# Performance work log

Measured on AMD Instinct MI355X. Metric: run time of the kernel, lower is better.

Reference implementation:

```python
import jax, jax.numpy as jnp
import numpy as np

B, N, D, H = 2, 2048, 1024, 16
HD = D // H
SCALE = 1.0 / float(np.sqrt(HD))


def _cx(r, i):
    return (r + 1j * i).astype(jnp.complex64)


def setup_inputs() -> dict:
    key = jax.random.key(0)
    ks = jax.random.split(key, 20)
    inp = {
        "Z_r": jax.random.normal(ks[0], (B, N, D), jnp.float32),
        "Z_i": jax.random.normal(ks[1], (B, N, D), jnp.float32),
    }
    i = 2
    w_scale = 0.02
    for nm in ("q", "k", "v", "o"):
        inp[f"w{nm}_r"] = jax.random.normal(ks[i], (D, D), jnp.float32) * w_scale
        inp[f"w{nm}_i"] = jax.random.normal(ks[i + 1], (D, D), jnp.float32) * w_scale
        inp[f"b{nm}_r"] = jax.random.normal(ks[i + 2], (D,), jnp.float32) * w_scale
        inp[f"b{nm}_i"] = jax.random.normal(ks[i + 3], (D,), jnp.float32) * w_scale
        i += 4
    inp["mask"] = jax.random.randint(ks[18], (B, N), 0, 2, jnp.int32)
    return inp


def reference(Z_r, Z_i, wq_r, wq_i, bq_r, bq_i, wk_r, wk_i, bk_r, bk_i,
              wv_r, wv_i, bv_r, bv_i, wo_r, wo_i, bo_r, bo_i, mask):
    Z = _cx(Z_r, Z_i)  # (B,N,D) complex64

    def lin(x, wr, wi, br, bi):  # complex nn.Linear: x @ W^T + b
        return x @ _cx(wr, wi).T + _cx(br, bi)

    def heads(x):  # (B,N,D) -> (B,H,N,HD)
        return x.reshape(B, N, H, HD).transpose(0, 2, 1, 3)

    q = heads(lin(Z, wq_r, wq_i, bq_r, bq_i))
    k = heads(lin(Z, wk_r, wk_i, bk_r, bk_i))
    v = heads(lin(Z, wv_r, wv_i, bv_r, bv_i))

    # Re(q @ k^T) with plain transpose (no conjugate), as in the torch code:
    # Re = qr.kr^T - qi.ki^T  (computed directly on real parts, no wasted imag GEMM)
    scores = (jnp.einsum('bhnd,bhmd->bhnm', q.real, k.real)
              - jnp.einsum('bhnd,bhmd->bhnm', q.imag, k.imag)) * SCALE
    scores = jnp.where(mask[:, None, None, :] == 0, jnp.float32(-1e9), scores)
    w = jax.nn.softmax(scores, axis=-1)  # (B,H,N,N) real

    # complex output: real weights times complex V -> apply to real/imag separately
    out_r = jnp.einsum('bhnm,bhmd->bhnd', w, v.real)
    out_i = jnp.einsum('bhnm,bhmd->bhnd', w, v.imag)
    out = _cx(out_r, out_i).transpose(0, 2, 1, 3).reshape(B, N, D)

    y = Z + lin(out, wo_r, wo_i, bo_r, bo_i)
    # return real/imag stacked as float32: (2,B,N,D)
    return jnp.stack([y.real, y.imag])
```

## Files before the change

kernel.cpp:

```cpp
#include <hip/hip_runtime.h>
#include <math.h>

#define BB 2
#define NN 2048
#define DD 1024
#define KA 2048
#define HH 16
#define HD 64
#define MM (BB*NN)
#define SCALE 0.125f

typedef __attribute__((ext_vector_type(8))) short bf16x8;
typedef __attribute__((ext_vector_type(4))) short bf16x4;
typedef __attribute__((ext_vector_type(4))) float f32x4;

#define MFMA(a,b,c) __builtin_amdgcn_mfma_f32_16x16x32_bf16(a,b,c,0,0,0)

__device__ __forceinline__ unsigned short f2bf(float x) {
    union { float f; unsigned u; } v; v.f = x;
    unsigned r = v.u + 0x7FFFu + ((v.u >> 16) & 1u);
    return (unsigned short)(r >> 16);
}

__device__ __forceinline__ void async16(void* l, const void* g) {
    __builtin_amdgcn_global_load_lds(
        (const __attribute__((address_space(1))) unsigned int*)g,
        (__attribute__((address_space(3))) unsigned int*)l, 16, 0, 0);
}

__device__ __forceinline__ bf16x8 ld8s(const short* p) {
    bf16x4 lo = *(const bf16x4*)p;
    bf16x4 hi = *(const bf16x4*)(p + 4);
    bf16x8 r;
    r[0]=lo[0]; r[1]=lo[1]; r[2]=lo[2]; r[3]=lo[3];
    r[4]=hi[0]; r[5]=hi[1]; r[6]=hi[2]; r[7]=hi[3];
    return r;
}
__device__ __forceinline__ void st8s(short* p, bf16x8 v) {
    bf16x4 lo, hi;
    lo[0]=v[0]; lo[1]=v[1]; lo[2]=v[2]; lo[3]=v[3];
    hi[0]=v[4]; hi[1]=v[5]; hi[2]=v[6]; hi[3]=v[7];
    *(bf16x4*)p = lo;
    *(bf16x4*)(p + 4) = hi;
}

__global__ __launch_bounds__(256) void mask_scan(const int* __restrict__ mask,
                                                 int* __restrict__ idxArr,
                                                 int* __restrict__ cntArr)
{
    const int b = blockIdx.x, t = threadIdx.x;
    __shared__ int part[256];
    int m[8]; int c = 0;
#pragma unroll
    for (int j = 0; j < 8; j++) { m[j] = mask[b*NN + t*8 + j]; c += (m[j] != 0); }
    part[t] = c; __syncthreads();
    for (int off = 1; off < 256; off <<= 1) {
        int v = (t >= off) ? part[t - off] : 0;
        __syncthreads();
        part[t] += v;
        __syncthreads();
    }
    int base = part[t] - c;
    int total = part[255];
#pragma unroll
    for (int j = 0; j < 8; j++) if (m[j]) idxArr[b*NN + base++] = t*8 + j;
    for (int p = total + t; p < NN; p += 256) idxArr[b*NN + p] = 0;
    if (t == 0) cntArr[b] = total;
}

__global__ __launch_bounds__(256) void cvt_aug(
    const float* __restrict__ Zr, const float* __restrict__ Zi,
    const float* __restrict__ wqr, const float* __restrict__ wqi,
    const float* __restrict__ wkr, const float* __restrict__ wki,
    const float* __restrict__ wvr, const float* __restrict__ wvi,
    const float* __restrict__ wor, const float* __restrict__ woi,
    unsigned short* __restrict__ Zaug,
    unsigned short* __restrict__ Wqa, unsigned short* __restrict__ Wka,
    unsigned short* __restrict__ Wva, unsigned short* __restrict__ Woa)
{
    const int bid = blockIdx.x, t = threadIdx.x;
    const int col = t * 8;
    const float* src;
    float sgn = 1.0f;
    unsigned short* dst;

    if (bid < 4096) {
        const int m = bid;
        src = (col < 1024) ? (Zr + (size_t)m*1024 + col) : (Zi + (size_t)m*1024 + col - 1024);
        dst = Zaug + (size_t)m * KA + col;
    } else {
        const int w = (bid - 4096) >> 11;
        const int r = (bid - 4096) & 2047;
        const int o = r & 1023;
        const float *wr_, *wi_;
        unsigned short* wa;
        switch (w) {
            case 0: wr_ = wqr; wi_ = wqi; wa = Wqa; break;
            case 1: wr_ = wkr; wi_ = wki; wa = Wka; break;
            case 2: wr_ = wvr; wi_ = wvi; wa = Wva; break;
            default: wr_ = wor; wi_ = woi; wa = Woa; break;
        }
        const bool imagrow = (r >= 1024);
        if (!imagrow) {
            if (col < 1024) { src = wr_ + (size_t)o*1024 + col; sgn = 1.0f; }
            else            { src = wi_ + (size_t)o*1024 + col - 1024; sgn = -1.0f; }
        } else {
            const float s = (w == 1) ? -1.0f : 1.0f;
            if (col < 1024) { src = wi_ + (size_t)o*1024 + col; sgn = s; }
            else            { src = wr_ + (size_t)o*1024 + col - 1024; sgn = s; }
        }
        dst = wa + (size_t)r * KA + col;
    }

    float4 a = *(const float4*)src;
    float4 b4 = *(const float4*)(src + 4);
    bf16x8 o8;
    o8[0]=(short)f2bf(sgn*a.x); o8[1]=(short)f2bf(sgn*a.y);
    o8[2]=(short)f2bf(sgn*a.z); o8[3]=(short)f2bf(sgn*a.w);
    o8[4]=(short)f2bf(sgn*b4.x); o8[5]=(short)f2bf(sgn*b4.y);
    o8[6]=(short)f2bf(sgn*b4.z); o8[7]=(short)f2bf(sgn*b4.w);
    *(bf16x8*)dst = o8;
}

__global__ __launch_bounds__(256) void proj_all(
    const unsigned short* __restrict__ Zaug,
    const unsigned short* __restrict__ Wqa, const unsigned short* __restrict__ Wka,
    const unsigned short* __restrict__ Wva,
    const float* __restrict__ bqr, const float* __restrict__ bqi,
    const float* __restrict__ bkr, const float* __restrict__ bki,
    const float* __restrict__ bvr, const float* __restrict__ bvi,
    const int* __restrict__ idxArr, const int* __restrict__ cntArr,
    unsigned short* __restrict__ Qr, unsigned short* __restrict__ Qi,
    unsigned short* __restrict__ Krc, unsigned short* __restrict__ nKic,
    unsigned short* __restrict__ Vtr, unsigned short* __restrict__ Vti)
{
    const int gx = blockIdx.x;
    int slice, b = 0, m0c;
    const unsigned short* wsel;
    const float *br, *bi;
    if (gx < 32) {
        slice = 0; m0c = gx * 128;
        wsel = Wqa; br = bqr; bi = bqi;
    } else if (gx < 64) {
        slice = 1; int t = gx - 32; b = t >> 4; m0c = (t & 15) * 128;
        wsel = Wka; br = bkr; bi = bki;
    } else {
        slice = 2; int t = gx - 64; b = t >> 4; m0c = (t & 15) * 128;
        wsel = Wva; br = bvr; bi = bvi;
    }
    if (slice != 0) {
        const int cnt = cntArr[b];
        if (m0c >= ((cnt + 63) & ~63)) return;
    }

    __shared__ __align__(16) short S[2][2][128][32];
    __shared__ int idx_s[128];

    const int tid = threadIdx.x;
    const int lane = tid & 63, wave = tid >> 6;
    const int lr = lane & 15, lg = lane >> 4;
    const int wrow = (wave >> 1) * 64, wcol = (wave & 1) * 64;
    const int o0 = blockIdx.y * 128;

    if (tid < 128)
        idx_s[tid] = (slice == 0) ? (m0c + tid) : (b*NN + idxArr[b*NN + m0c + tid]);
    __syncthreads();

    const int rsub = lane >> 2;
    const int colo = (lane & 3) * 8;

    const unsigned short* gp[4];
    gp[0] = Zaug + (size_t)idx_s[wave*16 + rsub] * KA + colo;
    gp[1] = Zaug + (size_t)idx_s[(wave + 4)*16 + rsub] * KA + colo;
    gp[2] = wsel + (size_t)(o0 + wave*16 + rsub) * KA + colo;
    gp[3] = wsel + (size_t)(o0 + 64 + wave*16 + rsub) * KA + colo;

    int lpo[4];
    lpo[0] = wave * 1024 + lane * 16;
    lpo[1] = (wave + 4) * 1024 + lane * 16;
    lpo[2] = 8192 + wave * 1024 + lane * 16;
    lpo[3] = 8192 + (wave + 4) * 1024 + lane * 16;

    f32x4 acc[4][4];
#pragma unroll
    for (int m = 0; m < 4; m++)
#pragma unroll
        for (int n = 0; n < 4; n++) acc[m][n] = (f32x4){0.f,0.f,0.f,0.f};

#pragma unroll
    for (int i = 0; i < 4; i++) { async16((char*)S + lpo[i], gp[i]); gp[i] += 32; }
    asm volatile("s_waitcnt vmcnt(0)" ::: "memory");
    __builtin_amdgcn_s_barrier();
    __builtin_amdgcn_sched_barrier(0);

    for (int t = 0; t < KA/32; t++) {
        const int cur = t & 1;
        char* nb = (char*)S + (cur ^ 1) * 16384;
#pragma unroll
        for (int i = 0; i < 4; i++) { async16(nb + lpo[i], gp[i]); gp[i] += 32; }

        const short (*Sa)[32] = (const short (*)[32])((const char*)S + cur * 16384);
        const short (*Sb)[32] = Sa + 128;
        bf16x8 af[4], bw[4];
#pragma unroll
        for (int m = 0; m < 4; m++) af[m] = *(const bf16x8*)&Sa[wrow + m*16 + lr][lg*8];
#pragma unroll
        for (int n = 0; n < 4; n++) bw[n] = *(const bf16x8*)&Sb[wcol + n*16 + lr][lg*8];
#pragma unroll
        for (int m = 0; m < 4; m++)
#pragma unroll
            for (int n = 0; n < 4; n++) acc[m][n] = MFMA(af[m], bw[n], acc[m][n]);

        asm volatile("s_waitcnt vmcnt(0)" ::: "memory");
        __builtin_amdgcn_s_barrier();
        __builtin_amdgcn_sched_barrier(0);
    }

#pragma unroll
    for (int mi = 0; mi < 4; mi++)
#pragma unroll
        for (int nj = 0; nj < 4; nj++) {
            const int o = o0 + wcol + nj*16 + lr;
            const int half = o >> 10;
            const int oc = o & 1023;
            const int h = oc >> 6, hd = oc & 63;
            const float bias = half ? ((slice == 1) ? -bi[oc] : bi[oc]) : br[oc];
            if (slice == 2) {
                bf16x4 p4;
#pragma unroll
                for (int reg = 0; reg < 4; reg++)
                    p4[reg] = (short)f2bf(acc[mi][nj][reg] + bias);
                const int jc = m0c + wrow + mi*16 + lg*4;
                size_t base = ((size_t)((b*HH + h)*HD + hd)) * NN + jc;
                if (half) *(bf16x4*)&Vti[base] = p4;
                else      *(bf16x4*)&Vtr[base] = p4;
            } else if (slice == 1) {
                unsigned short* dst = half ? nKic : Krc;
#pragma unroll
                for (int reg = 0; reg < 4; reg++) {
                    const int jc = m0c + wrow + mi*16 + lg*4 + reg;
                    dst[((size_t)((b*HH + h)*NN + jc)) * HD + hd] =
                        f2bf(acc[mi][nj][reg] + bias);
                }
            } else {
                unsigned short* dst = half ? Qi : Qr;
#pragma unroll
                for (int reg = 0; reg < 4; reg++) {
                    const int m = m0c + wrow + mi*16 + lg*4 + reg;
                    const int b2 = m >> 11, n = m & (NN - 1);
                    dst[((size_t)((b2*HH + h)*NN + n)) * HD + hd] =
                        f2bf((acc[mi][nj][reg] + bias) * SCALE);
                }
            }
        }
}

#define LDP 72
__global__ __launch_bounds__(256) void attn_mfma(
    const unsigned short* __restrict__ Qr, const unsigned short* __restrict__ Qi,
    const unsigned short* __restrict__ Krc, const unsigned short* __restrict__ nKic,
    const unsigned short* __restrict__ Vtc, const unsigned short* __restrict__ Vtic,
    const int* __restrict__ cntArr,
    unsigned short* __restrict__ Aaug)
{
    __shared__ short Kr_s[64][LDP], Ki_s[64][LDP], Vr_s[64][LDP], Vi_s[64][LDP];
    __shared__ short P_s[4][32][LDP];

    const int tid = threadIdx.x;
    const int lane = tid & 63, wave = tid >> 6;
    const int lr = lane & 15, lg = lane >> 4;
    const int h = blockIdx.y, b = blockIdx.z;
    const int n0 = blockIdx.x * 128 + wave * 32;
    const size_t qb = ((size_t)(b*HH + h)) * NN * HD;
    const int cnt = cntArr[b];
    const int ct = (cnt + 63) & ~63;

    bf16x8 qr[2][2], qi[2][2];
#pragma unroll
    for (int mf = 0; mf < 2; mf++)
#pragma unroll
        for (int kf = 0; kf < 2; kf++) {
            qr[mf][kf] = *(const bf16x8*)&Qr[qb + (size_t)(n0 + mf*16 + lr) * HD + kf*32 + lg*8];
            qi[mf][kf] = *(const bf16x8*)&Qi[qb + (size_t)(n0 + mf*16 + lr) * HD + kf*32 + lg*8];
        }

    f32x4 o_r[2][4], o_i[2][4];
#pragma unroll
    for (int mf = 0; mf < 2; mf++)
#pragma unroll
        for (int nf = 0; nf < 4; nf++) {
            o_r[mf][nf] = (f32x4){0.f,0.f,0.f,0.f};
            o_i[mf][nf] = (f32x4){0.f,0.f,0.f,0.f};
        }
    float m_run[2][4], l_run[2][4];
#pragma unroll
    for (int mf = 0; mf < 2; mf++)
#pragma unroll
        for (int r = 0; r < 4; r++) { m_run[mf][r] = -3.0e38f; l_run[mf][r] = 0.0f; }

    for (int t0 = 0; t0 < ct; t0 += 64) {
        __syncthreads();
        for (int c = tid; c < 512; c += 256) {
            int row = c >> 3, ch = (c & 7) * 8;
            st8s(&Kr_s[row][ch], *(const bf16x8*)&Krc [qb + (size_t)(t0 + row) * HD + ch]);
            st8s(&Ki_s[row][ch], *(const bf16x8*)&nKic[qb + (size_t)(t0 + row) * HD + ch]);
            st8s(&Vr_s[row][ch], *(const bf16x8*)&Vtc [qb + (size_t)row * NN + t0 + ch]);
            st8s(&Vi_s[row][ch], *(const bf16x8*)&Vtic[qb + (size_t)row * NN + t0 + ch]);
        }
        __syncthreads();

        f32x4 sacc[2][4];
#pragma unroll
        for (int nf = 0; nf < 4; nf++) {
            bf16x8 k0f = ld8s(&Kr_s[nf*16 + lr][lg*8]);
            bf16x8 k1f = ld8s(&Kr_s[nf*16 + lr][32 + lg*8]);
            bf16x8 i0f = ld8s(&Ki_s[nf*16 + lr][lg*8]);
            bf16x8 i1f = ld8s(&Ki_s[nf*16 + lr][32 + lg*8]);
#pragma unroll
            for (int mf = 0; mf < 2; mf++) {
                f32x4 a = (f32x4){0.f,0.f,0.f,0.f};
                a = MFMA(qr[mf][0], k0f, a);
                a = MFMA(qr[mf][1], k1f, a);
                a = MFMA(qi[mf][0], i0f, a);
                a = MFMA(qi[mf][1], i1f, a);
                sacc[mf][nf] = a;
            }
        }

        if (t0 + 64 > cnt) {
#pragma unroll
            for (int nf = 0; nf < 4; nf++) {
                if (t0 + nf*16 + lr >= cnt) {
#pragma unroll
                    for (int mf = 0; mf < 2; mf++)
#pragma unroll
                        for (int r = 0; r < 4; r++) sacc[mf][nf][r] = -1e9f;
                }
            }
        }

#pragma unroll
        for (int mf = 0; mf < 2; mf++) {
            float fac[4];
#pragma unroll
            for (int r = 0; r < 4; r++) {
                float v = fmaxf(fmaxf(sacc[mf][0][r], sacc[mf][1][r]),
                                fmaxf(sacc[mf][2][r], sacc[mf][3][r]));
                v = fmaxf(v, __shfl_xor(v, 1, 64));
                v = fmaxf(v, __shfl_xor(v, 2, 64));
                v = fmaxf(v, __shfl_xor(v, 4, 64));
                v = fmaxf(v, __shfl_xor(v, 8, 64));
                float mn = fmaxf(m_run[mf][r], v);
                fac[r] = __expf(m_run[mf][r] - mn);
                m_run[mf][r] = mn;
            }
            float psum[4] = {0.f, 0.f, 0.f, 0.f};
#pragma unroll
            for (int nf = 0; nf < 4; nf++)
#pragma unroll
                for (int r = 0; r < 4; r++) {
                    float p = __expf(sacc[mf][nf][r] - m_run[mf][r]);
                    psum[r] += p;
                    P_s[wave][mf*16 + lg*4 + r][nf*16 + lr] = (short)f2bf(p);
                }
#pragma unroll
            for (int r = 0; r < 4; r++) {
                float ps = psum[r];
                ps += __shfl_xor(ps, 1, 64);
                ps += __shfl_xor(ps, 2, 64);
                ps += __shfl_xor(ps, 4, 64);
                ps += __shfl_xor(ps, 8, 64);
                l_run[mf][r] = l_run[mf][r] * fac[r] + ps;
            }
#pragma unroll
            for (int nf = 0; nf < 4; nf++)
#pragma unroll
                for (int r = 0; r < 4; r++) {
                    o_r[mf][nf][r] *= fac[r];
                    o_i[mf][nf][r] *= fac[r];
                }
        }
        __syncthreads();

        bf16x8 pa[2][2];
#pragma unroll
        for (int mf = 0; mf < 2; mf++) {
            pa[mf][0] = ld8s(&P_s[wave][mf*16 + lr][lg*8]);
            pa[mf][1] = ld8s(&P_s[wave][mf*16 + lr][32 + lg*8]);
        }
#pragma unroll
        for (int nf = 0; nf < 4; nf++) {
            bf16x8 v0 = ld8s(&Vr_s[nf*16 + lr][lg*8]);
            bf16x8 v1 = ld8s(&Vr_s[nf*16 + lr][32 + lg*8]);
            bf16x8 w0 = ld8s(&Vi_s[nf*16 + lr][lg*8]);
            bf16x8 w1 = ld8s(&Vi_s[nf*16 + lr][32 + lg*8]);
#pragma unroll
            for (int mf = 0; mf < 2; mf++) {
                o_r[mf][nf] = MFMA(pa[mf][0], v0, o_r[mf][nf]);
                o_r[mf][nf] = MFMA(pa[mf][1], v1, o_r[mf][nf]);
                o_i[mf][nf] = MFMA(pa[mf][0], w0, o_i[mf][nf]);
                o_i[mf][nf] = MFMA(pa[mf][1], w1, o_i[mf][nf]);
            }
        }
    }

#pragma unroll
    for (int mf = 0; mf < 2; mf++) {
        float invl[4];
#pragma unroll
        for (int r = 0; r < 4; r++) invl[r] = 1.0f / l_run[mf][r];
#pragma unroll
        for (int nf = 0; nf < 4; nf++)
#pragma unroll
            for (int r = 0; r < 4; r++) {
                int row = n0 + mf*16 + lg*4 + r;
                int col = h*HD + nf*16 + lr;
                size_t o = ((size_t)(b*NN + row)) * KA + col;
                Aaug[o]        = f2bf(o_r[mf][nf][r] * invl[r]);
                Aaug[o + 1024] = f2bf(o_i[mf][nf][r] * invl[r]);
            }
    }
}

__global__ __launch_bounds__(256) void final_mfma(
    const unsigned short* __restrict__ Aaug, const unsigned short* __restrict__ Woa,
    const float* __restrict__ bor, const float* __restrict__ boi,
    const float* __restrict__ Zr, const float* __restrict__ Zi,
    float* __restrict__ out)
{
    __shared__ __align__(16) short S[2][2][128][32];

    const int tid = threadIdx.x;
    const int lane = tid & 63, wave = tid >> 6;
    const int lr = lane & 15, lg = lane >> 4;
    const int wrow = (wave >> 1) * 64, wcol = (wave & 1) * 64;
    const int m0 = blockIdx.x * 128, o0 = blockIdx.y * 128;

    const int rsub = lane >> 2;
    const int colo = (lane & 3) * 8;

    const unsigned short* gp[4];
    gp[0] = Aaug + (size_t)(m0 + wave*16 + rsub) * KA + colo;
    gp[1] = Aaug + (size_t)(m0 + 64 + wave*16 + rsub) * KA + colo;
    gp[2] = Woa + (size_t)(o0 + wave*16 + rsub) * KA + colo;
    gp[3] = Woa + (size_t)(o0 + 64 + wave*16 + rsub) * KA + colo;

    int lpo[4];
    lpo[0] = wave * 1024 + lane * 16;
    lpo[1] = (wave + 4) * 1024 + lane * 16;
    lpo[2] = 8192 + wave * 1024 + lane * 16;
    lpo[3] = 8192 + (wave + 4) * 1024 + lane * 16;

    f32x4 acc[4][4];
#pragma unroll
    for (int m = 0; m < 4; m++)
#pragma unroll
        for (int n = 0; n < 4; n++) acc[m][n] = (f32x4){0.f,0.f,0.f,0.f};

#pragma unroll
    for (int i = 0; i < 4; i++) { async16((char*)S + lpo[i], gp[i]); gp[i] += 32; }
    asm volatile("s_waitcnt vmcnt(0)" ::: "memory");
    __builtin_amdgcn_s_barrier();
    __builtin_amdgcn_sched_barrier(0);

    for (int t = 0; t < KA/32; t++) {
        const int cur = t & 1;
        char* nb = (char*)S + (cur ^ 1) * 16384;
#pragma unroll
        for (int i = 0; i < 4; i++) { async16(nb + lpo[i], gp[i]); gp[i] += 32; }

        const short (*Sa)[32] = (const short (*)[32])((const char*)S + cur * 16384);
        const short (*Sb)[32] = Sa + 128;
        bf16x8 af[4], bw[4];
#pragma unroll
        for (int m = 0; m < 4; m++) af[m] = *(const bf16x8*)&Sa[wrow + m*16 + lr][lg*8];
#pragma unroll
        for (int n = 0; n < 4; n++) bw[n] = *(const bf16x8*)&Sb[wcol + n*16 + lr][lg*8];
#pragma unroll
        for (int m = 0; m < 4; m++)
#pragma unroll
            for (int n = 0; n < 4; n++) acc[m][n] = MFMA(af[m], bw[n], acc[m][n]);

        asm volatile("s_waitcnt vmcnt(0)" ::: "memory");
        __builtin_amdgcn_s_barrier();
        __builtin_amdgcn_sched_barrier(0);
    }

#pragma unroll
    for (int mi = 0; mi < 4; mi++)
#pragma unroll
        for (int nj = 0; nj < 4; nj++) {
            const int o = o0 + wcol + nj*16 + lr;
            const int half = o >> 10;
            const int oc = o & 1023;
            const float bias = half ? boi[oc] : bor[oc];
            const float* resid = half ? Zi : Zr;
            float* dst = out + (half ? (size_t)MM * DD : 0);
#pragma unroll
            for (int reg = 0; reg < 4; reg++) {
                const int m = m0 + wrow + mi*16 + lg*4 + reg;
                size_t zi = (size_t)m * DD + oc;
                dst[zi] = acc[mi][nj][reg] + bias + resid[zi];
            }
        }
}

extern "C" void kernel_launch(void* const* d_in, const int* in_sizes, int n_in,
                              void* d_out, int out_size, void* d_ws, size_t ws_size,
                              hipStream_t stream)
{
    const float* Zr  = (const float*)d_in[0];
    const float* Zi  = (const float*)d_in[1];
    const float* wqr = (const float*)d_in[2];
    const float* wqi = (const float*)d_in[3];
    const float* bqr = (const float*)d_in[4];
    const float* bqi = (const float*)d_in[5];
    const float* wkr = (const float*)d_in[6];
    const float* wki = (const float*)d_in[7];
    const float* bkr = (const float*)d_in[8];
    const float* bki = (const float*)d_in[9];
    const float* wvr = (const float*)d_in[10];
    const float* wvi = (const float*)d_in[11];
    const float* bvr = (const float*)d_in[12];
    const float* bvi = (const float*)d_in[13];
    const float* wor = (const float*)d_in[14];
    const float* woi = (const float*)d_in[15];
    const float* bor = (const float*)d_in[16];
    const float* boi = (const float*)d_in[17];
    const int*  mask = (const int*)d_in[18];

    unsigned short* w16 = (unsigned short*)d_ws;
    const size_t ZA = (size_t)MM * KA;
    const size_t WA = (size_t)KA * KA;
    const size_t HN = (size_t)MM * DD;
    unsigned short* Zaug = w16;
    unsigned short* Wqa  = Zaug + ZA;
    unsigned short* Wka  = Wqa + WA;
    unsigned short* Wva  = Wka + WA;
    unsigned short* Woa  = Wva + WA;
    unsigned short* Qr16 = Woa + WA;
    unsigned short* Qi16 = Qr16 + HN;
    unsigned short* Krc16 = Qi16 + HN;
    unsigned short* nKic16 = Krc16 + HN;
    unsigned short* Vtr16 = nKic16 + HN;
    unsigned short* Vti16 = Vtr16 + HN;
    unsigned short* Aaug = Vti16 + HN;
    int* idxArr = (int*)(Aaug + ZA);
    int* cntArr = idxArr + BB * NN;

    mask_scan<<<BB, 256, 0, stream>>>(mask, idxArr, cntArr);

    cvt_aug<<<12288, 256, 0, stream>>>(
        Zr, Zi, wqr, wqi, wkr, wki, wvr, wvi, wor, woi,
        Zaug, Wqa, Wka, Wva, Woa);

    proj_all<<<dim3(96, 16), 256, 0, stream>>>(
        Zaug, Wqa, Wka, Wva,
        bqr, bqi, bkr, bki, bvr, bvi, idxArr, cntArr,
        Qr16, Qi16, Krc16, nKic16, Vtr16, Vti16);

    attn_mfma<<<dim3(NN/128, HH, BB), 256, 0, stream>>>(
        Qr16, Qi16, Krc16, nKic16, Vtr16, Vti16, cntArr, Aaug);

    final_mfma<<<dim3(32, 16), 256, 0, stream>>>(
        Aaug, Woa, bor, boi, Zr, Zi, (float*)d_out);
}
```

Measured before the change: 309.5 us.

## Triple-buffer LDS in projection GEMMs with XOR-swizzled tiles to avoid bank conflicts

After: 266.3 us. -14.0%, faster.

```diff
diff --git a/kernel.cpp b/kernel.cpp
--- a/kernel.cpp
+++ b/kernel.cpp
@@ -9,6 +9,7 @@
 #define HD 64
 #define MM (BB*NN)
 #define SCALE 0.125f
+#define NT (KA/32)
 
 typedef __attribute__((ext_vector_type(8))) short bf16x8;
 typedef __attribute__((ext_vector_type(4))) short bf16x4;
@@ -153,7 +154,7 @@
         if (m0c >= ((cnt + 63) & ~63)) return;
     }
 
-    __shared__ __align__(16) short S[2][2][128][32];
+    __shared__ __align__(16) short S[3][2][128][32];
     __shared__ int idx_s[128];
 
     const int tid = threadIdx.x;
@@ -167,19 +168,23 @@
     __syncthreads();
 
     const int rsub = lane >> 2;
-    const int colo = (lane & 3) * 8;
+    const int csrc = (((lane & 3) ^ ((lane >> 3) & 3)) * 8);
 
     const unsigned short* gp[4];
-    gp[0] = Zaug + (size_t)idx_s[wave*16 + rsub] * KA + colo;
-    gp[1] = Zaug + (size_t)idx_s[(wave + 4)*16 + rsub] * KA + colo;
-    gp[2] = wsel + (size_t)(o0 + wave*16 + rsub) * KA + colo;
-    gp[3] = wsel + (size_t)(o0 + 64 + wave*16 + rsub) * KA + colo;
-
     int lpo[4];
-    lpo[0] = wave * 1024 + lane * 16;
-    lpo[1] = (wave + 4) * 1024 + lane * 16;
-    lpo[2] = 8192 + wave * 1024 + lane * 16;
-    lpo[3] = 8192 + (wave + 4) * 1024 + lane * 16;
+#pragma unroll
+    for (int i = 0; i < 4; i++) {
+        const int s = i * 4 + wave;
+        if (s < 8) {
+            const int row = s * 16 + rsub;
+            gp[i] = Zaug + (size_t)idx_s[row] * KA + csrc;
+            lpo[i] = s * 1024 + lane * 16;
+        } else {
+            const int row = (s - 8) * 16 + rsub;
+            gp[i] = wsel + (size_t)(o0 + row) * KA + csrc;
+            lpo[i] = 8192 + (s - 8) * 1024 + lane * 16;
+        }
+    }
 
     f32x4 acc[4][4];
 #pragma unroll
@@ -189,31 +194,53 @@
 
 #pragma unroll
     for (int i = 0; i < 4; i++) { async16((char*)S + lpo[i], gp[i]); gp[i] += 32; }
+#pragma unroll
+    for (int i = 0; i < 4; i++) { async16((char*)S + 16384 + lpo[i], gp[i]); gp[i] += 32; }
+
+    const int kb = ((lg ^ ((lr >> 1) & 3)) * 8);
+
+    int cur = 0, stg = 2;
+    for (int t = 0; t < NT - 1; t++) {
+        asm volatile("s_waitcnt vmcnt(4)" ::: "memory");
+        __builtin_amdgcn_s_barrier();
+        __builtin_amdgcn_sched_barrier(0);
+
+        if (t + 2 < NT) {
+            char* nb = (char*)S + stg * 16384;
+#pragma unroll
+            for (int i = 0; i < 4; i++) { async16(nb + lpo[i], gp[i]); gp[i] += 32; }
+        }
+
+        const short (*Sa)[32] = (const short (*)[32])((const char*)S + cur * 16384);
+        const short (*Sb)[32] = Sa + 128;
+        bf16x8 af[4], bw[4];
+#pragma unroll
+        for (int m = 0; m < 4; m++) af[m] = *(const bf16x8*)&Sa[wrow + m*16 + lr][kb];
+#pragma unroll
+        for (int n = 0; n < 4; n++) bw[n] = *(const bf16x8*)&Sb[wcol + n*16 + lr][kb];
+#pragma unroll
+        for (int m = 0; m < 4; m++)
+#pragma unroll
+            for (int n = 0; n < 4; n++) acc[m][n] = MFMA(af[m], bw[n], acc[m][n]);
+
+        cur = (cur == 2) ? 0 : cur + 1;
+        stg = (stg == 2) ? 0 : stg + 1;
+    }
     asm volatile("s_waitcnt vmcnt(0)" ::: "memory");
     __builtin_amdgcn_s_barrier();
     __builtin_amdgcn_sched_barrier(0);
-
-    for (int t = 0; t < KA/32; t++) {
-        const int cur = t & 1;
-        char* nb = (char*)S + (cur ^ 1) * 16384;
-#pragma unroll
-        for (int i = 0; i < 4; i++) { async16(nb + lpo[i], gp[i]); gp[i] += 32; }
-
+    {
         const short (*Sa)[32] = (const short (*)[32])((const char*)S + cur * 16384);
         const short (*Sb)[32] = Sa + 128;
         bf16x8 af[4], bw[4];
 #pragma unroll
-        for (int m = 0; m < 4; m++) af[m] = *(const bf16x8*)&Sa[wrow + m*16 + lr][lg*8];
-#pragma unroll
-        for (int n = 0; n < 4; n++) bw[n] = *(const bf16x8*)&Sb[wcol + n*16 + lr][lg*8];
+        for (int m = 0; m < 4; m++) af[m] = *(const bf16x8*)&Sa[wrow + m*16 + lr][kb];
+#pragma unroll
+        for (int n = 0; n < 4; n++) bw[n] = *(const bf16x8*)&Sb[wcol + n*16 + lr][kb];
 #pragma unroll
         for (int m = 0; m < 4; m++)
 #pragma unroll
             for (int n = 0; n < 4; n++) acc[m][n] = MFMA(af[m], bw[n], acc[m][n]);
-
-        asm volatile("s_waitcnt vmcnt(0)" ::: "memory");
-        __builtin_amdgcn_s_barrier();
-        __builtin_amdgcn_sched_barrier(0);
     }
 
 #pragma unroll
@@ -428,7 +455,7 @@
     const float* __restrict__ Zr, const float* __restrict__ Zi,
     float* __restrict__ out)
 {
-    __shared__ __align__(16) short S[2][2][128][32];
+    __shared__ __align__(16) short S[3][2][128][32];
 
     const int tid = threadIdx.x;
     const int lane = tid & 63, wave = tid >> 6;
@@ -437,19 +464,23 @@
     const int m0 = blockIdx.x * 128, o0 = blockIdx.y * 128;
 
     const int rsub = lane >> 2;
-    const int colo = (lane & 3) * 8;
+    const int csrc = (((lane & 3) ^ ((lane >> 3) & 3)) * 8);
 
     const unsigned short* gp[4];
-    gp[0] = Aaug + (size_t)(m0 + wave*16 + rsub) * KA + colo;
-    gp[1] = Aaug + (size_t)(m0 + 64 + wave*16 + rsub) * KA + colo;
-    gp[2] = Woa + (size_t)(o0 + wave*16 + rsub) * KA + colo;
-    gp[3] = Woa + (size_t)(o0 + 64 + wave*16 + rsub) * KA + colo;
-
     int lpo[4];
-    lpo[0] = wave * 1024 + lane * 16;
-    lpo[1] = (wave + 4) * 1024 + lane * 16;
-    lpo[2] = 8192 + wave * 1024 + lane * 16;
-    lpo[3] = 8192 + (wave + 4) * 1024 + lane * 16;
+#pragma unroll
+    for (int i = 0; i < 4; i++) {
+        const int s = i * 4 + wave;
+        if (s < 8) {
+            const int row = s * 16 + rsub;
+            gp[i] = Aaug + (size_t)(m0 + row) * KA + csrc;
+            lpo[i] = s * 1024 + lane * 16;
+        } else {
+            const int row = (s - 8) * 16 + rsub;
+            gp[i] = Woa + (size_t)(o0 + row) * KA + csrc;
+            lpo[i] = 8192 + (s - 8) * 1024 + lane * 16;
+        }
+    }
 
     f32x4 acc[4][4];
 #pragma unroll
@@ -459,31 +490,53 @@
 
 #pragma unroll
     for (int i = 0; i < 4; i++) { async16((char*)S + lpo[i], gp[i]); gp[i] += 32; }
+#pragma unroll
+    for (int i = 0; i < 4; i++) { async16((char*)S + 16384 + lpo[i], gp[i]); gp[i] += 32; }
+
+    const int kb = ((lg ^ ((lr >> 1) & 3)) * 8);
+
+    int cur = 0, stg = 2;
+    for (int t = 0; t < NT - 1; t++) {
+        asm volatile("s_waitcnt vmcnt(4)" ::: "memory");
+        __builtin_amdgcn_s_barrier();
+        __builtin_amdgcn_sched_barrier(0);
+
+        if (t + 2 < NT) {
+            char* nb = (char*)S + stg * 16384;
+#pragma unroll
+            for (int i = 0; i < 4; i++) { async16(nb + lpo[i], gp[i]); gp[i] += 32; }
+        }
+
+        const short (*Sa)[32] = (const short (*)[32])((const char*)S + cur * 16384);
+        const short (*Sb)[32] = Sa + 128;
+        bf16x8 af[4], bw[4];
+#pragma unroll
+        for (int m = 0; m < 4; m++) af[m] = *(const bf16x8*)&Sa[wrow + m*16 + lr][kb];
+#pragma unroll
+        for (int n = 0; n < 4; n++) bw[n] = *(const bf16x8*)&Sb[wcol + n*16 + lr][kb];
+#pragma unroll
+        for (int m = 0; m < 4; m++)
+#pragma unroll
+            for (int n = 0; n < 4; n++) acc[m][n] = MFMA(af[m], bw[n], acc[m][n]);
+
+        cur = (cur == 2) ? 0 : cur + 1;
+        stg = (stg == 2) ? 0 : stg + 1;
+    }
     asm volatile("s_waitcnt vmcnt(0)" ::: "memory");
     __builtin_amdgcn_s_barrier();
     __builtin_amdgcn_sched_barrier(0);
-
-    for (int t = 0; t < KA/32; t++) {
-        const int cur = t & 1;
-        char* nb = (char*)S + (cur ^ 1) * 16384;
-#pragma unroll
-        for (int i = 0; i < 4; i++) { async16(nb + lpo[i], gp[i]); gp[i] += 32; }
-
+    {
         const short (*Sa)[32] = (const short (*)[32])((const char*)S + cur * 16384);
         const short (*Sb)[32] = Sa + 128;
         bf16x8 af[4], bw[4];
 #pragma unroll
-        for (int m = 0; m < 4; m++) af[m] = *(const bf16x8*)&Sa[wrow + m*16 + lr][lg*8];
-#pragma unroll
-        for (int n = 0; n < 4; n++) bw[n] = *(const bf16x8*)&Sb[wcol + n*16 + lr][lg*8];
+        for (int m = 0; m < 4; m++) af[m] = *(const bf16x8*)&Sa[wrow + m*16 + lr][kb];
+#pragma unroll
+        for (int n = 0; n < 4; n++) bw[n] = *(const bf16x8*)&Sb[wcol + n*16 + lr][kb];
 #pragma unroll
         for (int m = 0; m < 4; m++)
 #pragma unroll
             for (int n = 0; n < 4; n++) acc[m][n] = MFMA(af[m], bw[n], acc[m][n]);
-
-        asm volatile("s_waitcnt vmcnt(0)" ::: "memory");
-        __builtin_amdgcn_s_barrier();
-        __builtin_amdgcn_sched_barrier(0);
     }
 
 #pragma unroll
```
